# Performance work log

Hardware: AMD Instinct MI355X
Metric: run time of the kernel (lower is better)

## Reference

```python
import jax, jax.numpy as jnp
import numpy as np

CHANNELS = 256   # input_channels == output_channels == res_feature channels
HIDDEN = 128
NODES = 7

def setup_inputs() -> dict:
    key = jax.random.key(0)
    k1, k2, k3, k4, k5 = jax.random.split(key, 5)
    batch, d, h, w = 2, 16, 64, 64
    inp = jax.random.normal(k1, (1, batch, NODES, HIDDEN), dtype=jnp.float32)
    res_feature = jax.random.normal(k2, (batch, CHANNELS, d, h, w), dtype=jnp.float32)
    # xavier_uniform-style init
    def xavier(k, shape):
        fan_in, fan_out = shape[0], shape[1]
        a = jnp.sqrt(6.0 / (fan_in + fan_out))
        return jax.random.uniform(k, shape, dtype=jnp.float32, minval=-a, maxval=a)
    node_fea_for_res = xavier(k3, (CHANNELS, NODES))
    node_fea_for_hidden = xavier(k4, (HIDDEN, 1))
    weight = xavier(k5, (HIDDEN, CHANNELS))
    return {"inp": inp, "res_feature": res_feature,
            "node_fea_for_res": node_fea_for_res,
            "node_fea_for_hidden": node_fea_for_hidden,
            "weight": weight}

def reference(inp, res_feature, node_fea_for_res, node_fea_for_hidden, weight):
    b, c, d, h, w = res_feature.shape
    # [b, dhw, c]
    rf = res_feature.reshape(b, c, d * h * w).transpose(0, 2, 1)
    # scores from residual features: [b, dhw, nodes]
    n1 = rf @ node_fea_for_res
    # scores from node hidden features (constant over spatial dim): [b, nodes]
    # (original expands input over dhw then matmuls with [hidden,1]; equivalent)
    n2 = (inp[0] @ node_fea_for_hidden)[..., 0]
    attn = jax.nn.softmax(n1 + n2[:, None, :], axis=-1)  # [b, dhw, nodes]
    new_weight = inp[0] @ weight                          # [b, nodes, c]
    feature_out = jnp.einsum('bpn,bnc->bpc', attn, new_weight)  # [b, dhw, c]
    feature_out = feature_out.transpose(0, 2, 1).reshape(b, c, d, h, w)
    return jax.nn.relu(feature_out)
```

## Files before the change

kernel.cpp:

```cpp
#include <hip/hip_runtime.h>

#define DHW   65536
#define NCH   256
#define NNODE 7
#define NHID  128
#define NBATCH 2

__global__ void prep_kernel(const float* __restrict__ inp,
                            const float* __restrict__ nfh,
                            const float* __restrict__ weight,
                            float* __restrict__ nwt,
                            float* __restrict__ n2g)
{
    const int bn = blockIdx.x;
    const int b  = bn / NNODE;
    const int n  = bn % NNODE;
    const int t  = threadIdx.x;
    const float* ih = inp + (b * NNODE + n) * NHID;

    float acc = 0.f;
    #pragma unroll 8
    for (int h = 0; h < NHID; ++h)
        acc = fmaf(ih[h], weight[h * NCH + t], acc);
    nwt[(b * NCH + t) * 8 + n] = acc;

    __shared__ float red[NHID];
    if (t < NHID) red[t] = ih[t] * nfh[t];
    __syncthreads();
    for (int s = NHID / 2; s > 0; s >>= 1) {
        if (t < s) red[t] += red[t + s];
        __syncthreads();
    }
    if (t == 0) n2g[b * 8 + n] = red[0];
}

__global__ __launch_bounds__(256, 2)
void main_kernel(const float* __restrict__ rf,
                 const float* __restrict__ w1,
                 const float* __restrict__ nwt,
                 const float* __restrict__ n2g,
                 float* __restrict__ out)
{
    __shared__ float4 w1_lds[NCH][2];
    __shared__ float4 nw_lds[NCH][2];
    __shared__ float  n2_lds[8];

    const int t   = threadIdx.x;
    const int blk = blockIdx.x;
    const int b   = blk >> 8;
    const int p   = ((blk & 255) << 8) + t;

    {
        const float* src = w1 + t * NNODE;
        float* dst = (float*)&w1_lds[t][0];
        #pragma unroll
        for (int n = 0; n < NNODE; ++n) dst[n] = src[n];
        dst[7] = 0.f;
    }
    {
        const float4* src = (const float4*)(nwt + b * NCH * 8);
        float4* dst = &nw_lds[0][0];
        dst[t]       = src[t];
        dst[t + 256] = src[t + 256];
    }
    if (t < 8) n2_lds[t] = (t < NNODE) ? n2g[b * 8 + t] : 0.f;
    __syncthreads();

    const float* rp = rf + ((size_t)(b * NCH) << 16) + p;
    float s0 = n2_lds[0], s1 = n2_lds[1], s2 = n2_lds[2], s3 = n2_lds[3];
    float s4 = n2_lds[4], s5 = n2_lds[5], s6 = n2_lds[6];
    #pragma unroll 8
    for (int c = 0; c < NCH; ++c) {
        float v = rp[(size_t)c << 16];
        float4 wa = w1_lds[c][0];
        float4 wb = w1_lds[c][1];
        s0 = fmaf(v, wa.x, s0);
        s1 = fmaf(v, wa.y, s1);
        s2 = fmaf(v, wa.z, s2);
        s3 = fmaf(v, wa.w, s3);
        s4 = fmaf(v, wb.x, s4);
        s5 = fmaf(v, wb.y, s5);
        s6 = fmaf(v, wb.z, s6);
    }

    float m = fmaxf(fmaxf(fmaxf(s0, s1), fmaxf(s2, s3)),
                    fmaxf(fmaxf(s4, s5), s6));
    float e0 = __expf(s0 - m), e1 = __expf(s1 - m), e2 = __expf(s2 - m);
    float e3 = __expf(s3 - m), e4 = __expf(s4 - m), e5 = __expf(s5 - m);
    float e6 = __expf(s6 - m);
    float inv = 1.0f / (e0 + e1 + e2 + e3 + e4 + e5 + e6);
    float a0 = e0 * inv, a1 = e1 * inv, a2 = e2 * inv, a3 = e3 * inv;
    float a4 = e4 * inv, a5 = e5 * inv, a6 = e6 * inv;

    float* op = out + ((size_t)(b * NCH) << 16) + p;
    #pragma unroll 8
    for (int c = 0; c < NCH; ++c) {
        float4 na = nw_lds[c][0];
        float4 nb = nw_lds[c][1];
        float o = a0 * na.x + a1 * na.y + a2 * na.z + a3 * na.w
                + a4 * nb.x + a5 * nb.y + a6 * nb.z;
        op[(size_t)c << 16] = fmaxf(o, 0.f);
    }
}

extern "C" void kernel_launch(void* const* d_in, const int* in_sizes, int n_in,
                              void* d_out, int out_size, void* d_ws, size_t ws_size,
                              hipStream_t stream) {
    const float* inp = (const float*)d_in[0];
    const float* rf  = (const float*)d_in[1];
    const float* w1  = (const float*)d_in[2];
    const float* nfh = (const float*)d_in[3];
    const float* wgt = (const float*)d_in[4];
    float* out = (float*)d_out;

    float* nwt = (float*)d_ws;
    float* n2g = nwt + NBATCH * NCH * 8;

    prep_kernel<<<NBATCH * NNODE, 256, 0, stream>>>(inp, nfh, wgt, nwt, n2g);
    main_kernel<<<NBATCH * 256, 256, 0, stream>>>(rf, w1, nwt, n2g, out);
}
```

Measured before the change: 255.0 us.

## Split channel reduction across wavefronts with LDS combine, drop LDS weight staging

Each block now covers 64 spatial positions, and its four wavefronts each reduce a quarter of the 256 channels. Partial scores are combined through shared memory before the softmax, and each wave then writes its own 64 output channels. Weights are pre-padded in the prep kernel and read straight from global memory with wave-uniform addresses instead of being staged in LDS. The aim is more blocks and higher occupancy (launch bounds 8) so that memory latency is hidden on this bandwidth-bound kernel. In exchange it adds a barrier and a shared-memory reduction per block.

```diff
diff --git a/kernel.cpp b/kernel.cpp
--- a/kernel.cpp
+++ b/kernel.cpp
@@ -1,16 +1,18 @@
 #include <hip/hip_runtime.h>
 
-#define DHW   65536
-#define NCH   256
-#define NNODE 7
-#define NHID  128
+#define DHW    65536
+#define NCH    256
+#define NNODE  7
+#define NHID   128
 #define NBATCH 2
 
 __global__ void prep_kernel(const float* __restrict__ inp,
                             const float* __restrict__ nfh,
                             const float* __restrict__ weight,
+                            const float* __restrict__ w1,
                             float* __restrict__ nwt,
-                            float* __restrict__ n2g)
+                            float* __restrict__ n2g,
+                            float* __restrict__ w1p)
 {
     const int bn = blockIdx.x;
     const int b  = bn / NNODE;
@@ -24,6 +26,12 @@
         acc = fmaf(ih[h], weight[h * NCH + t], acc);
     nwt[(b * NCH + t) * 8 + n] = acc;
 
+    if (bn == 0) {
+        #pragma unroll
+        for (int n2 = 0; n2 < NNODE; ++n2) w1p[t * 8 + n2] = w1[t * NNODE + n2];
+        w1p[t * 8 + 7] = 0.f;
+    }
+
     __shared__ float red[NHID];
     if (t < NHID) red[t] = ih[t] * nfh[t];
     __syncthreads();
@@ -34,46 +42,32 @@
     if (t == 0) n2g[b * 8 + n] = red[0];
 }
 
-__global__ __launch_bounds__(256, 2)
+__global__ __launch_bounds__(256, 8)
 void main_kernel(const float* __restrict__ rf,
-                 const float* __restrict__ w1,
+                 const float* __restrict__ w1p,
                  const float* __restrict__ nwt,
                  const float* __restrict__ n2g,
                  float* __restrict__ out)
 {
-    __shared__ float4 w1_lds[NCH][2];
-    __shared__ float4 nw_lds[NCH][2];
-    __shared__ float  n2_lds[8];
+    __shared__ float red[8][4][64];
 
-    const int t   = threadIdx.x;
-    const int blk = blockIdx.x;
-    const int b   = blk >> 8;
-    const int p   = ((blk & 255) << 8) + t;
+    const int t    = threadIdx.x;
+    const int lane = t & 63;
+    const int wv   = __builtin_amdgcn_readfirstlane(t >> 6);
+    const int blk  = blockIdx.x;
+    const int b    = blk >> 10;
+    const int p    = ((blk & 1023) << 6) + lane;
+    const int c0   = wv << 6;
 
-    {
-        const float* src = w1 + t * NNODE;
-        float* dst = (float*)&w1_lds[t][0];
-        #pragma unroll
-        for (int n = 0; n < NNODE; ++n) dst[n] = src[n];
-        dst[7] = 0.f;
-    }
-    {
-        const float4* src = (const float4*)(nwt + b * NCH * 8);
-        float4* dst = &nw_lds[0][0];
-        dst[t]       = src[t];
-        dst[t + 256] = src[t + 256];
-    }
-    if (t < 8) n2_lds[t] = (t < NNODE) ? n2g[b * 8 + t] : 0.f;
-    __syncthreads();
+    const float*  rp = rf + ((size_t)b << 24) + ((size_t)c0 << 16) + p;
+    const float4* wq = (const float4*)w1p + (c0 << 1);
 
-    const float* rp = rf + ((size_t)(b * NCH) << 16) + p;
-    float s0 = n2_lds[0], s1 = n2_lds[1], s2 = n2_lds[2], s3 = n2_lds[3];
-    float s4 = n2_lds[4], s5 = n2_lds[5], s6 = n2_lds[6];
+    float s0 = 0.f, s1 = 0.f, s2 = 0.f, s3 = 0.f, s4 = 0.f, s5 = 0.f, s6 = 0.f;
     #pragma unroll 8
-    for (int c = 0; c < NCH; ++c) {
-        float v = rp[(size_t)c << 16];
-        float4 wa = w1_lds[c][0];
-        float4 wb = w1_lds[c][1];
+    for (int c = 0; c < 64; ++c) {
+        float  v  = rp[(size_t)c << 16];
+        float4 wa = wq[c * 2];
+        float4 wb = wq[c * 2 + 1];
         s0 = fmaf(v, wa.x, s0);
         s1 = fmaf(v, wa.y, s1);
         s2 = fmaf(v, wa.z, s2);
@@ -83,20 +77,35 @@
         s6 = fmaf(v, wb.z, s6);
     }
 
-    float m = fmaxf(fmaxf(fmaxf(s0, s1), fmaxf(s2, s3)),
-                    fmaxf(fmaxf(s4, s5), s6));
-    float e0 = __expf(s0 - m), e1 = __expf(s1 - m), e2 = __expf(s2 - m);
-    float e3 = __expf(s3 - m), e4 = __expf(s4 - m), e5 = __expf(s5 - m);
-    float e6 = __expf(s6 - m);
+    red[0][wv][lane] = s0;  red[1][wv][lane] = s1;  red[2][wv][lane] = s2;
+    red[3][wv][lane] = s3;  red[4][wv][lane] = s4;  red[5][wv][lane] = s5;
+    red[6][wv][lane] = s6;
+    __syncthreads();
+
+    const float* n2 = n2g + b * 8;
+    float r0 = red[0][0][lane] + red[0][1][lane] + red[0][2][lane] + red[0][3][lane] + n2[0];
+    float r1 = red[1][0][lane] + red[1][1][lane] + red[1][2][lane] + red[1][3][lane] + n2[1];
+    float r2 = red[2][0][lane] + red[2][1][lane] + red[2][2][lane] + red[2][3][lane] + n2[2];
+    float r3 = red[3][0][lane] + red[3][1][lane] + red[3][2][lane] + red[3][3][lane] + n2[3];
+    float r4 = red[4][0][lane] + red[4][1][lane] + red[4][2][lane] + red[4][3][lane] + n2[4];
+    float r5 = red[5][0][lane] + red[5][1][lane] + red[5][2][lane] + red[5][3][lane] + n2[5];
+    float r6 = red[6][0][lane] + red[6][1][lane] + red[6][2][lane] + red[6][3][lane] + n2[6];
+
+    float m = fmaxf(fmaxf(fmaxf(r0, r1), fmaxf(r2, r3)),
+                    fmaxf(fmaxf(r4, r5), r6));
+    float e0 = __expf(r0 - m), e1 = __expf(r1 - m), e2 = __expf(r2 - m);
+    float e3 = __expf(r3 - m), e4 = __expf(r4 - m), e5 = __expf(r5 - m);
+    float e6 = __expf(r6 - m);
     float inv = 1.0f / (e0 + e1 + e2 + e3 + e4 + e5 + e6);
     float a0 = e0 * inv, a1 = e1 * inv, a2 = e2 * inv, a3 = e3 * inv;
     float a4 = e4 * inv, a5 = e5 * inv, a6 = e6 * inv;
 
-    float* op = out + ((size_t)(b * NCH) << 16) + p;
+    const float4* nq = (const float4*)nwt + ((b * NCH + c0) << 1);
+    float* op = out + ((size_t)b << 24) + ((size_t)c0 << 16) + p;
     #pragma unroll 8
-    for (int c = 0; c < NCH; ++c) {
-        float4 na = nw_lds[c][0];
-        float4 nb = nw_lds[c][1];
+    for (int c = 0; c < 64; ++c) {
+        float4 na = nq[c * 2];
+        float4 nb = nq[c * 2 + 1];
         float o = a0 * na.x + a1 * na.y + a2 * na.z + a3 * na.w
                 + a4 * nb.x + a5 * nb.y + a6 * nb.z;
         op[(size_t)c << 16] = fmaxf(o, 0.f);
@@ -115,7 +124,8 @@
 
     float* nwt = (float*)d_ws;
     float* n2g = nwt + NBATCH * NCH * 8;
+    float* w1p = n2g + NBATCH * 8;
 
-    prep_kernel<<<NBATCH * NNODE, 256, 0, stream>>>(inp, nfh, wgt, nwt, n2g);
-    main_kernel<<<NBATCH * 256, 256, 0, stream>>>(rf, w1, nwt, n2g, out);
+    prep_kernel<<<NBATCH * NNODE, 256, 0, stream>>>(inp, nfh, wgt, w1, nwt, n2g, w1p);
+    main_kernel<<<NBATCH * 1024, 256, 0, stream>>>(rf, w1p, nwt, n2g, out);
 }
```

Measured after the change: 266.2 us. 1.04x slower.
